# Performance work log

Hardware: AMD Instinct MI355X
Metric: run time of the kernel (lower is better)

The kernel has to match this reference:

```python
import jax, jax.numpy as jnp
import numpy as np

D_MODEL = 1024
NUM_HEADS = 16
D_K = D_MODEL // NUM_HEADS


def setup_inputs() -> dict:
    key = jax.random.key(0)
    ks = jax.random.split(key, 11)
    B, S, D = 2, 2048, D_MODEL
    scale = 1.0 / np.sqrt(D)
    inp = {
        'q': jax.random.normal(ks[0], (B, S, D), jnp.float32),
        'k': jax.random.normal(ks[1], (B, S, D), jnp.float32),
        'v': jax.random.normal(ks[2], (B, S, D), jnp.float32),
        # torch nn.Linear weights are [out, in]; y = x @ W.T + b
        'Wq': jax.random.normal(ks[3], (D, D), jnp.float32) * scale,
        'bq': jax.random.normal(ks[4], (D,), jnp.float32) * scale,
        'Wk': jax.random.normal(ks[5], (D, D), jnp.float32) * scale,
        'bk': jax.random.normal(ks[6], (D,), jnp.float32) * scale,
        'Wv': jax.random.normal(ks[7], (D, D), jnp.float32) * scale,
        'bv': jax.random.normal(ks[8], (D,), jnp.float32) * scale,
        'Wo': jax.random.normal(ks[9], (D, D), jnp.float32) * scale,
        'bo': jax.random.normal(ks[10], (D,), jnp.float32) * scale,
    }
    return inp


def reference(q, k, v, Wq, bq, Wk, bk, Wv, bv, Wo, bo):
    B, S, D = q.shape
    H, dk = NUM_HEADS, D_K

    def proj(x, W, b):
        # torch Linear: x @ W.T + b ; then [B,S,H,dk] -> [B,H,S,dk]
        y = jnp.einsum('bsd,ed->bse', x, W) + b
        return y.reshape(B, S, H, dk).transpose(0, 2, 1, 3)

    Q = proj(q, Wq, bq)
    K = proj(k, Wk, bk)
    V = proj(v, Wv, bv)

    # NOTE: original module omits the 1/sqrt(d_k) scaling — faithful here.
    scores = jnp.einsum('bhqd,bhkd->bhqk', Q, K)  # [B,H,S,S]
    attn = jax.nn.softmax(scores, axis=-1)
    out = jnp.einsum('bhqk,bhkd->bhqd', attn, V)  # [B,H,S,dk]
    out = out.transpose(0, 2, 1, 3).reshape(B, S, D)
    return jnp.einsum('bsd,ed->bse', out, Wo) + bo
```

## Files before the change

kernel.cpp:

```cpp
#include <hip/hip_runtime.h>
#include <hip/hip_bf16.h>
#include <stdint.h>


using bf16 = __hip_bfloat16;
typedef __attribute__((ext_vector_type(8))) short v8s;
typedef __attribute__((ext_vector_type(4))) float v4f;

#define NB_ ((size_t)4194304)
#define ND_ ((size_t)1048576)

__device__ __forceinline__ void async16(const void* g, void* l) {
  __builtin_amdgcn_global_load_lds(
      (const __attribute__((address_space(1))) unsigned int*)g,
      (__attribute__((address_space(3))) unsigned int*)l, 16, 0, 0);
}

__device__ __forceinline__ v4f mfma16(v8s a, v8s b, v4f c) {
  return __builtin_amdgcn_mfma_f32_16x16x32_bf16(a, b, c, 0, 0, 0);
}

struct SplitArgs {
  const float4* src[7];
  ushort4* hi[7];
  ushort4* lo[7];
  int n4[7];
};

__global__ __launch_bounds__(256) void splitk(SplitArgs sa) {
  const int z = blockIdx.y;
  const float4* __restrict__ src = sa.src[z];
  ushort4* __restrict__ dh = sa.hi[z];
  ushort4* __restrict__ dl = sa.lo[z];
  const int n4 = sa.n4[z];
  const int stride = gridDim.x * blockDim.x;
  for (int i = blockIdx.x * blockDim.x + threadIdx.x; i < n4; i += stride) {
    const float4 x = src[i];
    float vals[4] = {x.x, x.y, x.z, x.w};
    unsigned short hs[4], ls[4];
#pragma unroll
    for (int j = 0; j < 4; ++j) {
      bf16 hb = __float2bfloat16(vals[j]);
      float rest = vals[j] - __bfloat162float(hb);
      bf16 lb = __float2bfloat16(rest);
      __builtin_memcpy(&hs[j], &hb, 2);
      __builtin_memcpy(&ls[j], &lb, 2);
    }
    ushort4 hv; hv.x = hs[0]; hv.y = hs[1]; hv.z = hs[2]; hv.w = hs[3];
    ushort4 lv; lv.x = ls[0]; lv.y = ls[1]; lv.z = ls[2]; lv.w = ls[3];
    dh[i] = hv;
    dl[i] = lv;
  }
}

struct GemmArgs {
  const bf16* Ah[3];
  const bf16* Al[3];
  const bf16* Bh[3];
  const bf16* Bl[3];
  const float* bias[3];
  void* O0[3];
  void* O1[3];
  int mode[3];
};

template <int TM>
__global__ __launch_bounds__(256, TM == 128 ? 3 : 2) void gemm3t(GemmArgs ga) {
  constexpr int MFR = TM / 32;
  const int z = blockIdx.z;
  const bf16* __restrict__ Ah = ga.Ah[z];
  const bf16* __restrict__ Al = ga.Al[z];
  const bf16* __restrict__ Bh = ga.Bh[z];
  const bf16* __restrict__ Bl = ga.Bl[z];
  const float* __restrict__ bias = ga.bias[z];
  const int mode = ga.mode[z];

  __shared__ alignas(16) bf16 lA0[TM * 32];
  __shared__ alignas(16) bf16 lA1[TM * 32];
  __shared__ alignas(16) bf16 lB0[128 * 32];
  __shared__ alignas(16) bf16 lB1[128 * 32];

  const int tid = threadIdx.x;
  const int lane = tid & 63;
  const int w = tid >> 6, wr = w >> 1, wc = w & 1;
  const int ln = lane & 15, g = lane >> 4;
  const int h4 = g * 4;
  const int m0 = blockIdx.y * TM, n0 = blockIdx.x * 128;

  v4f acc[MFR][4];
#pragma unroll
  for (int i = 0; i < MFR; ++i)
#pragma unroll
    for (int j = 0; j < 4; ++j)
#pragma unroll
      for (int r = 0; r < 4; ++r) acc[i][j][r] = 0.f;

  for (int k0 = 0; k0 < 1024; k0 += 32) {
#pragma unroll
    for (int p = 0; p < TM / 64; ++p) {
      const int idx = p * 256 + tid;
      const int row = idx >> 2, c = idx & 3;
      const int cs = (c ^ (row & 3)) * 8;
      const size_t gA = (size_t)(m0 + row) * 1024 + k0 + cs;
      async16(Ah + gA, &lA0[idx * 8]);
      async16(Al + gA, &lA1[idx * 8]);
    }
#pragma unroll
    for (int p = 0; p < 2; ++p) {
      const int idx = p * 256 + tid;
      const int row = idx >> 2, c = idx & 3;
      const int cs = (c ^ (row & 3)) * 8;
      const size_t gB = (size_t)(n0 + row) * 1024 + k0 + cs;
      async16(Bh + gB, &lB0[idx * 8]);
      async16(Bl + gB, &lB1[idx * 8]);
    }
    __syncthreads();

    const char* pA0 = (const char*)lA0;
    const char* pA1 = (const char*)lA1;
    const char* pB0 = (const char*)lB0;
    const char* pB1 = (const char*)lB1;

    v8s a0[MFR], a1[MFR], b0[4], b1[4];
#pragma unroll
    for (int f = 0; f < MFR; ++f) {
      const int row = wr * (TM / 2) + f * 16 + ln;
      const int off = (row << 6) + ((g ^ (row & 3)) << 4);
      a0[f] = *(const v8s*)(pA0 + off);
      a1[f] = *(const v8s*)(pA1 + off);
    }
#pragma unroll
    for (int f = 0; f < 4; ++f) {
      const int row = wc * 64 + f * 16 + ln;
      const int off = (row << 6) + ((g ^ (row & 3)) << 4);
      b0[f] = *(const v8s*)(pB0 + off);
      b1[f] = *(const v8s*)(pB1 + off);
    }
    __builtin_amdgcn_s_setprio(1);
#pragma unroll
    for (int i = 0; i < MFR; ++i)
#pragma unroll
      for (int j = 0; j < 4; ++j) {
        acc[i][j] = mfma16(a0[i], b0[j], acc[i][j]);
        acc[i][j] = mfma16(a0[i], b1[j], acc[i][j]);
        acc[i][j] = mfma16(a1[i], b0[j], acc[i][j]);
      }
    __builtin_amdgcn_s_setprio(0);
    __syncthreads();
  }

#pragma unroll
  for (int i = 0; i < MFR; ++i)
#pragma unroll
    for (int j = 0; j < 4; ++j) {
      const int col = n0 + wc * 64 + j * 16 + ln;
      const float bb = bias[col];
#pragma unroll
      for (int r = 0; r < 4; ++r) {
        const int row = m0 + wr * (TM / 2) + i * 16 + h4 + r;
        const float vv = acc[i][j][r] + bb;
        if (mode == 2) {
          ((float*)ga.O0[z])[(size_t)row * 1024 + col] = vv;
        } else {
          const int b_ = row >> 11, s_ = row & 2047;
          const int hh = col >> 6, dd = col & 63;
          if (mode == 0) {
            const size_t o = (((size_t)(b_ * 16 + hh)) * 2048 + s_) * 64 + dd;
            bf16 hb = __float2bfloat16(vv);
            ((bf16*)ga.O0[z])[o] = hb;
            ((bf16*)ga.O1[z])[o] = __float2bfloat16(vv - __bfloat162float(hb));
          } else {
            const size_t o = (((size_t)(b_ * 16 + hh)) * 64 + dd) * 2048 + s_;
            ((bf16*)ga.O0[z])[o] = __float2bfloat16(vv);
          }
        }
      }
    }
}

__global__ __launch_bounds__(256, 2) void attnk(
    const bf16* __restrict__ Qh, const bf16* __restrict__ Ql,
    const bf16* __restrict__ Kh, const bf16* __restrict__ Kl,
    const bf16* __restrict__ Vt,
    bf16* __restrict__ Oh, bf16* __restrict__ Ol) {
  __shared__ alignas(16) bf16 lKh[2][64 * 64];
  __shared__ alignas(16) bf16 lKl[2][64 * 64];
  __shared__ alignas(16) bf16 lVt[2][64 * 64];
  __shared__ alignas(16) bf16 lP[4][32 * 72];

  const int tid = threadIdx.x;
  const int lane = tid & 63, w = tid >> 6;
  const int ln = lane & 15, g = lane >> 4;
  const int h8 = g * 8, h4 = g * 4;
  const int bh = blockIdx.y;
  const int q0 = blockIdx.x * 128 + w * 32;

  v8s qh[2][2], ql[2][2];
#pragma unroll
  for (int mf = 0; mf < 2; ++mf) {
    const size_t rowg = (size_t)bh * 2048 + q0 + mf * 16 + ln;
#pragma unroll
    for (int ks = 0; ks < 2; ++ks) {
      qh[mf][ks] = *(const v8s*)&Qh[rowg * 64 + ks * 32 + h8];
      ql[mf][ks] = *(const v8s*)&Ql[rowg * 64 + ks * 32 + h8];
    }
  }

  v4f O[2][4];
  float lpart[2][4];
#pragma unroll
  for (int mf = 0; mf < 2; ++mf) {
#pragma unroll
    for (int r = 0; r < 4; ++r) lpart[mf][r] = 0.f;
#pragma unroll
    for (int d = 0; d < 4; ++d)
#pragma unroll
      for (int r = 0; r < 4; ++r) O[mf][d][r] = 0.f;
  }

  auto stage = [&](int buf, int kv0) {
#pragma unroll
    for (int p = 0; p < 2; ++p) {
      const int idx = p * 256 + tid;
      const int row = idx >> 3;
      const int cs = ((idx & 7) ^ (row & 7)) * 8;
      const size_t gk = ((size_t)bh * 2048 + kv0 + row) * 64 + cs;
      async16(Kh + gk, &lKh[buf][idx * 8]);
      async16(Kl + gk, &lKl[buf][idx * 8]);
      const size_t gv = ((size_t)bh * 64 + row) * 2048 + kv0 + cs;
      async16(Vt + gv, &lVt[buf][idx * 8]);
    }
  };

  stage(0, 0);
  __syncthreads();

  for (int t = 0; t < 32; ++t) {
    const int cur = t & 1;
    if (t < 31) stage(cur ^ 1, (t + 1) * 64);

    v4f sacc[2][4];
#pragma unroll
    for (int mf = 0; mf < 2; ++mf)
#pragma unroll
      for (int kvf = 0; kvf < 4; ++kvf)
#pragma unroll
        for (int r = 0; r < 4; ++r) sacc[mf][kvf][r] = 0.f;

    const char* kbh = (const char*)&lKh[cur][0];
    const char* kbl = (const char*)&lKl[cur][0];
    const char* vbb = (const char*)&lVt[cur][0];

#pragma unroll
    for (int ks = 0; ks < 2; ++ks) {
      const int cbyte = (ks << 6) + (g << 4);
      v8s kh[4], kl[4];
#pragma unroll
      for (int kvf = 0; kvf < 4; ++kvf) {
        const int kr = kvf * 16 + ln;
        const int koff = (kr << 7) + (cbyte ^ ((kr & 7) << 4));
        kh[kvf] = *(const v8s*)(kbh + koff);
        kl[kvf] = *(const v8s*)(kbl + koff);
      }
      __builtin_amdgcn_s_setprio(1);
#pragma unroll
      for (int mf = 0; mf < 2; ++mf)
#pragma unroll
        for (int kvf = 0; kvf < 4; ++kvf) {
          sacc[mf][kvf] = mfma16(qh[mf][ks], kh[kvf], sacc[mf][kvf]);
          sacc[mf][kvf] = mfma16(qh[mf][ks], kl[kvf], sacc[mf][kvf]);
          sacc[mf][kvf] = mfma16(ql[mf][ks], kh[kvf], sacc[mf][kvf]);
        }
      __builtin_amdgcn_s_setprio(0);
    }

#pragma unroll
    for (int mf = 0; mf < 2; ++mf)
#pragma unroll
      for (int kvf = 0; kvf < 4; ++kvf)
#pragma unroll
        for (int r = 0; r < 4; ++r) {
          const float p = __expf(sacc[mf][kvf][r]);
          lpart[mf][r] += p;
          lP[w][(mf * 16 + h4 + r) * 72 + kvf * 16 + ln] = __float2bfloat16(p);
        }

#pragma unroll
    for (int ks = 0; ks < 2; ++ks) {
      const int cbyte = (ks << 6) + (g << 4);
      v8s pa[2], vb[4];
#pragma unroll
      for (int mf = 0; mf < 2; ++mf)
        pa[mf] = *(const v8s*)&lP[w][(mf * 16 + ln) * 72 + ks * 32 + h8];
#pragma unroll
      for (int dkf = 0; dkf < 4; ++dkf) {
        const int vr = dkf * 16 + ln;
        const int voff = (vr << 7) + (cbyte ^ ((vr & 7) << 4));
        vb[dkf] = *(const v8s*)(vbb + voff);
      }
      __builtin_amdgcn_s_setprio(1);
#pragma unroll
      for (int mf = 0; mf < 2; ++mf)
#pragma unroll
        for (int dkf = 0; dkf < 4; ++dkf)
          O[mf][dkf] = mfma16(pa[mf], vb[dkf], O[mf][dkf]);
      __builtin_amdgcn_s_setprio(0);
    }
    __syncthreads();
  }

  float lrow[2][4];
#pragma unroll
  for (int mf = 0; mf < 2; ++mf)
#pragma unroll
    for (int r = 0; r < 4; ++r) {
      float s = lpart[mf][r];
      s += __shfl_xor(s, 1, 64);
      s += __shfl_xor(s, 2, 64);
      s += __shfl_xor(s, 4, 64);
      s += __shfl_xor(s, 8, 64);
      lrow[mf][r] = s;
    }

  const int b_ = bh >> 4, hh = bh & 15;
#pragma unroll
  for (int mf = 0; mf < 2; ++mf)
#pragma unroll
    for (int r = 0; r < 4; ++r) {
      const float inv = 1.f / lrow[mf][r];
      const int s_ = blockIdx.x * 128 + w * 32 + mf * 16 + h4 + r;
#pragma unroll
      for (int dkf = 0; dkf < 4; ++dkf) {
        const float o = O[mf][dkf][r] * inv;
        const size_t off = ((size_t)b_ * 2048 + s_) * 1024 + hh * 64 + dkf * 16 + ln;
        bf16 hb = __float2bfloat16(o);
        Oh[off] = hb;
        Ol[off] = __float2bfloat16(o - __bfloat162float(hb));
      }
    }
}

extern "C" void kernel_launch(void* const* d_in, const int* in_sizes, int n_in,
                              void* d_out, int out_size, void* d_ws, size_t ws_size,
                              hipStream_t stream) {
  const float* q  = (const float*)d_in[0];
  const float* k  = (const float*)d_in[1];
  const float* v  = (const float*)d_in[2];
  const float* Wq = (const float*)d_in[3];
  const float* bq = (const float*)d_in[4];
  const float* Wk = (const float*)d_in[5];
  const float* bk = (const float*)d_in[6];
  const float* Wv = (const float*)d_in[7];
  const float* bv = (const float*)d_in[8];
  const float* Wo = (const float*)d_in[9];
  const float* bo = (const float*)d_in[10];

  const size_t NB = NB_, ND = ND_;
  bf16* P = (bf16*)d_ws;

  const bool fused = (ws_size >= (size_t)120 * 1024 * 1024);

  if (fused) {
    bf16 *qh = P, *ql = qh + NB, *kh = ql + NB, *kl = kh + NB, *vh = kl + NB, *vl = vh + NB;
    bf16 *wqh = vl + NB, *wql = wqh + ND, *wkh = wql + ND, *wkl = wkh + ND;
    bf16 *wvh = wkl + ND, *wvl = wvh + ND, *woh = wvl + ND, *wol = woh + ND;
    bf16 *Qh = wol + ND, *Ql = Qh + NB, *Kh2 = Ql + NB, *Kl2 = Kh2 + NB, *Vt = Kl2 + NB;
    bf16 *Ah = qh, *Al = ql;

    SplitArgs sa{};
    const float* srcs[7] = {q, k, v, Wq, Wk, Wv, Wo};
    bf16* his[7] = {qh, kh, vh, wqh, wkh, wvh, woh};
    bf16* los[7] = {ql, kl, vl, wql, wkl, wvl, wol};
    for (int i = 0; i < 7; ++i) {
      sa.src[i] = (const float4*)srcs[i];
      sa.hi[i] = (ushort4*)his[i];
      sa.lo[i] = (ushort4*)los[i];
      sa.n4[i] = (int)((i < 3 ? NB : ND) / 4);
    }
    splitk<<<dim3(512, 7), 256, 0, stream>>>(sa);

    GemmArgs ga{};
    ga.Ah[0] = qh; ga.Al[0] = ql; ga.Bh[0] = wqh; ga.Bl[0] = wql;
    ga.bias[0] = bq; ga.O0[0] = Qh; ga.O1[0] = Ql; ga.mode[0] = 0;
    ga.Ah[1] = kh; ga.Al[1] = kl; ga.Bh[1] = wkh; ga.Bl[1] = wkl;
    ga.bias[1] = bk; ga.O0[1] = Kh2; ga.O1[1] = Kl2; ga.mode[1] = 0;
    ga.Ah[2] = vh; ga.Al[2] = vl; ga.Bh[2] = wvh; ga.Bl[2] = wvl;
    ga.bias[2] = bv; ga.O0[2] = Vt; ga.O1[2] = nullptr; ga.mode[2] = 1;
    gemm3t<128><<<dim3(8, 32, 3), 256, 0, stream>>>(ga);

    attnk<<<dim3(16, 32), 256, 0, stream>>>(Qh, Ql, Kh2, Kl2, Vt, Ah, Al);

    GemmArgs go{};
    go.Ah[0] = Ah; go.Al[0] = Al; go.Bh[0] = woh; go.Bl[0] = wol;
    go.bias[0] = bo; go.O0[0] = d_out; go.O1[0] = nullptr; go.mode[0] = 2;
    gemm3t<64><<<dim3(8, 64, 1), 256, 0, stream>>>(go);
  } else {
    bf16 *ash = P, *asl = ash + NB, *wsh = asl + NB, *wsl = wsh + ND;
    bf16 *Qh = wsl + ND, *Ql = Qh + NB, *Kh2 = Ql + NB, *Kl2 = Kh2 + NB, *Vt = Kl2 + NB;

    auto do_split2 = [&](const float* a, const float* wsrc) {
      SplitArgs s{};
      s.src[0] = (const float4*)a; s.hi[0] = (ushort4*)ash; s.lo[0] = (ushort4*)asl;
      s.n4[0] = (int)(NB / 4);
      s.src[1] = (const float4*)wsrc; s.hi[1] = (ushort4*)wsh; s.lo[1] = (ushort4*)wsl;
      s.n4[1] = (int)(ND / 4);
      splitk<<<dim3(512, 2), 256, 0, stream>>>(s);
    };
    auto do_gemm = [&](const float* bias, void* o0, void* o1, int mode) {
      GemmArgs g{};
      g.Ah[0] = ash; g.Al[0] = asl; g.Bh[0] = wsh; g.Bl[0] = wsl;
      g.bias[0] = bias; g.O0[0] = o0; g.O1[0] = o1; g.mode[0] = mode;
      gemm3t<128><<<dim3(8, 32, 1), 256, 0, stream>>>(g);
    };

    do_split2(q, Wq); do_gemm(bq, Qh, Ql, 0);
    do_split2(k, Wk); do_gemm(bk, Kh2, Kl2, 0);
    do_split2(v, Wv); do_gemm(bv, Vt, nullptr, 1);

    attnk<<<dim3(16, 32), 256, 0, stream>>>(Qh, Ql, Kh2, Kl2, Vt, ash, asl);

    SplitArgs s4{};
    s4.src[0] = (const float4*)Wo; s4.hi[0] = (ushort4*)wsh; s4.lo[0] = (ushort4*)wsl;
    s4.n4[0] = (int)(ND / 4);
    splitk<<<dim3(512, 1), 256, 0, stream>>>(s4);
    GemmArgs g4{};
    g4.Ah[0] = ash; g4.Al[0] = asl; g4.Bh[0] = wsh; g4.Bl[0] = wsl;
    g4.bias[0] = bo; g4.O0[0] = d_out; g4.O1[0] = nullptr; g4.mode[0] = 2;
    gemm3t<64><<<dim3(8, 64, 1), 256, 0, stream>>>(g4);
  }
}
```

Measured before the change: 325.0 us.

## Restructure attention to 16-row waves with register-shuffled P; drop weight-lo term in V/O GEMMs

The attention kernel now uses 512 threads, with each wave owning 16 query rows instead of 32. It computes S transposed (K as the A operand), so the exponentiated probabilities can be passed into the PV MFMA through cross-lane shuffles rather than an LDS round-trip, and the per-wave P buffer in shared memory is gone. This is meant to cut LDS traffic and register pressure and to raise occupancy. Separately, the GEMM gains a per-problem term count, so the V projection and output projection skip the A_hi*B_lo MFMA and its weight-lo load, trading a small amount of precision for fewer MFMAs and less bandwidth.

```diff
diff --git a/kernel.cpp b/kernel.cpp
--- a/kernel.cpp
+++ b/kernel.cpp
@@ -6,6 +6,8 @@
 using bf16 = __hip_bfloat16;
 typedef __attribute__((ext_vector_type(8))) short v8s;
 typedef __attribute__((ext_vector_type(4))) float v4f;
+typedef __attribute__((ext_vector_type(4))) unsigned int v4u;
+union PW { v4u u; v8s s; };
 
 #define NB_ ((size_t)4194304)
 #define ND_ ((size_t)1048576)
@@ -18,6 +20,13 @@
 
 __device__ __forceinline__ v4f mfma16(v8s a, v8s b, v4f c) {
   return __builtin_amdgcn_mfma_f32_16x16x32_bf16(a, b, c, 0, 0, 0);
+}
+
+__device__ __forceinline__ unsigned short bfbits(float x) {
+  bf16 h = __float2bfloat16(x);
+  unsigned short u;
+  __builtin_memcpy(&u, &h, 2);
+  return u;
 }
 
 struct SplitArgs {
@@ -42,9 +51,8 @@
     for (int j = 0; j < 4; ++j) {
       bf16 hb = __float2bfloat16(vals[j]);
       float rest = vals[j] - __bfloat162float(hb);
-      bf16 lb = __float2bfloat16(rest);
-      __builtin_memcpy(&hs[j], &hb, 2);
-      __builtin_memcpy(&ls[j], &lb, 2);
+      hs[j] = bfbits(vals[j]);
+      ls[j] = bfbits(rest);
     }
     ushort4 hv; hv.x = hs[0]; hv.y = hs[1]; hv.z = hs[2]; hv.w = hs[3];
     ushort4 lv; lv.x = ls[0]; lv.y = ls[1]; lv.z = ls[2]; lv.w = ls[3];
@@ -62,6 +70,7 @@
   void* O0[3];
   void* O1[3];
   int mode[3];
+  int terms[3];
 };
 
 template <int TM>
@@ -74,6 +83,7 @@
   const bf16* __restrict__ Bl = ga.Bl[z];
   const float* __restrict__ bias = ga.bias[z];
   const int mode = ga.mode[z];
+  const bool nt3 = (ga.terms[z] == 3);
 
   __shared__ alignas(16) bf16 lA0[TM * 32];
   __shared__ alignas(16) bf16 lA1[TM * 32];
@@ -112,7 +122,7 @@
       const int cs = (c ^ (row & 3)) * 8;
       const size_t gB = (size_t)(n0 + row) * 1024 + k0 + cs;
       async16(Bh + gB, &lB0[idx * 8]);
-      async16(Bl + gB, &lB1[idx * 8]);
+      if (nt3) async16(Bl + gB, &lB1[idx * 8]);
     }
     __syncthreads();
 
@@ -134,7 +144,14 @@
       const int row = wc * 64 + f * 16 + ln;
       const int off = (row << 6) + ((g ^ (row & 3)) << 4);
       b0[f] = *(const v8s*)(pB0 + off);
-      b1[f] = *(const v8s*)(pB1 + off);
+    }
+    if (nt3) {
+#pragma unroll
+      for (int f = 0; f < 4; ++f) {
+        const int row = wc * 64 + f * 16 + ln;
+        const int off = (row << 6) + ((g ^ (row & 3)) << 4);
+        b1[f] = *(const v8s*)(pB1 + off);
+      }
     }
     __builtin_amdgcn_s_setprio(1);
 #pragma unroll
@@ -142,9 +159,15 @@
 #pragma unroll
       for (int j = 0; j < 4; ++j) {
         acc[i][j] = mfma16(a0[i], b0[j], acc[i][j]);
-        acc[i][j] = mfma16(a0[i], b1[j], acc[i][j]);
         acc[i][j] = mfma16(a1[i], b0[j], acc[i][j]);
       }
+    if (nt3) {
+#pragma unroll
+      for (int i = 0; i < MFR; ++i)
+#pragma unroll
+        for (int j = 0; j < 4; ++j)
+          acc[i][j] = mfma16(a0[i], b1[j], acc[i][j]);
+    }
     __builtin_amdgcn_s_setprio(0);
     __syncthreads();
   }
@@ -178,7 +201,7 @@
     }
 }
 
-__global__ __launch_bounds__(256, 2) void attnk(
+__global__ __launch_bounds__(512, 4) void attnk(
     const bf16* __restrict__ Qh, const bf16* __restrict__ Ql,
     const bf16* __restrict__ Kh, const bf16* __restrict__ Kl,
     const bf16* __restrict__ Vt,
@@ -186,70 +209,59 @@
   __shared__ alignas(16) bf16 lKh[2][64 * 64];
   __shared__ alignas(16) bf16 lKl[2][64 * 64];
   __shared__ alignas(16) bf16 lVt[2][64 * 64];
-  __shared__ alignas(16) bf16 lP[4][32 * 72];
 
   const int tid = threadIdx.x;
   const int lane = tid & 63, w = tid >> 6;
   const int ln = lane & 15, g = lane >> 4;
-  const int h8 = g * 8, h4 = g * 4;
+  const int h8 = g * 8;
   const int bh = blockIdx.y;
-  const int q0 = blockIdx.x * 128 + w * 32;
-
-  v8s qh[2][2], ql[2][2];
-#pragma unroll
-  for (int mf = 0; mf < 2; ++mf) {
-    const size_t rowg = (size_t)bh * 2048 + q0 + mf * 16 + ln;
-#pragma unroll
-    for (int ks = 0; ks < 2; ++ks) {
-      qh[mf][ks] = *(const v8s*)&Qh[rowg * 64 + ks * 32 + h8];
-      ql[mf][ks] = *(const v8s*)&Ql[rowg * 64 + ks * 32 + h8];
-    }
-  }
-
-  v4f O[2][4];
-  float lpart[2][4];
-#pragma unroll
-  for (int mf = 0; mf < 2; ++mf) {
-#pragma unroll
-    for (int r = 0; r < 4; ++r) lpart[mf][r] = 0.f;
-#pragma unroll
-    for (int d = 0; d < 4; ++d)
-#pragma unroll
-      for (int r = 0; r < 4; ++r) O[mf][d][r] = 0.f;
-  }
-
+  const int q0 = blockIdx.x * 128 + w * 16;
+
+  v8s qh[2], ql[2];
+  {
+    const size_t rowg = (size_t)bh * 2048 + q0 + ln;
+    qh[0] = *(const v8s*)&Qh[rowg * 64 + h8];
+    qh[1] = *(const v8s*)&Qh[rowg * 64 + 32 + h8];
+    ql[0] = *(const v8s*)&Ql[rowg * 64 + h8];
+    ql[1] = *(const v8s*)&Ql[rowg * 64 + 32 + h8];
+  }
+
+  v4f O[4];
+  float lpart = 0.f;
+#pragma unroll
+  for (int d = 0; d < 4; ++d)
+#pragma unroll
+    for (int r = 0; r < 4; ++r) O[d][r] = 0.f;
+
+  const int srow = tid >> 3, sc = tid & 7;
+  const int scs = (sc ^ (srow & 7)) * 8;
   auto stage = [&](int buf, int kv0) {
-#pragma unroll
-    for (int p = 0; p < 2; ++p) {
-      const int idx = p * 256 + tid;
-      const int row = idx >> 3;
-      const int cs = ((idx & 7) ^ (row & 7)) * 8;
-      const size_t gk = ((size_t)bh * 2048 + kv0 + row) * 64 + cs;
-      async16(Kh + gk, &lKh[buf][idx * 8]);
-      async16(Kl + gk, &lKl[buf][idx * 8]);
-      const size_t gv = ((size_t)bh * 64 + row) * 2048 + kv0 + cs;
-      async16(Vt + gv, &lVt[buf][idx * 8]);
-    }
+    const size_t gk = ((size_t)bh * 2048 + kv0 + srow) * 64 + scs;
+    async16(Kh + gk, &lKh[buf][tid * 8]);
+    async16(Kl + gk, &lKl[buf][tid * 8]);
+    const size_t gv = ((size_t)bh * 64 + srow) * 2048 + kv0 + scs;
+    async16(Vt + gv, &lVt[buf][tid * 8]);
   };
 
   stage(0, 0);
   __syncthreads();
+
+  const int sA = ln + ((g & 1) << 5);
+  const bool hiK = (g >> 1) != 0;
 
   for (int t = 0; t < 32; ++t) {
     const int cur = t & 1;
     if (t < 31) stage(cur ^ 1, (t + 1) * 64);
 
-    v4f sacc[2][4];
-#pragma unroll
-    for (int mf = 0; mf < 2; ++mf)
-#pragma unroll
-      for (int kvf = 0; kvf < 4; ++kvf)
-#pragma unroll
-        for (int r = 0; r < 4; ++r) sacc[mf][kvf][r] = 0.f;
-
     const char* kbh = (const char*)&lKh[cur][0];
     const char* kbl = (const char*)&lKl[cur][0];
     const char* vbb = (const char*)&lVt[cur][0];
+
+    v4f sacc[4];
+#pragma unroll
+    for (int kvf = 0; kvf < 4; ++kvf)
+#pragma unroll
+      for (int r = 0; r < 4; ++r) sacc[kvf][r] = 0.f;
 
 #pragma unroll
     for (int ks = 0; ks < 2; ++ks) {
@@ -264,34 +276,42 @@
       }
       __builtin_amdgcn_s_setprio(1);
 #pragma unroll
-      for (int mf = 0; mf < 2; ++mf)
-#pragma unroll
-        for (int kvf = 0; kvf < 4; ++kvf) {
-          sacc[mf][kvf] = mfma16(qh[mf][ks], kh[kvf], sacc[mf][kvf]);
-          sacc[mf][kvf] = mfma16(qh[mf][ks], kl[kvf], sacc[mf][kvf]);
-          sacc[mf][kvf] = mfma16(ql[mf][ks], kh[kvf], sacc[mf][kvf]);
-        }
+      for (int kvf = 0; kvf < 4; ++kvf) {
+        sacc[kvf] = mfma16(kh[kvf], qh[ks], sacc[kvf]);
+        sacc[kvf] = mfma16(kl[kvf], qh[ks], sacc[kvf]);
+        sacc[kvf] = mfma16(kh[kvf], ql[ks], sacc[kvf]);
+      }
       __builtin_amdgcn_s_setprio(0);
     }
 
-#pragma unroll
-    for (int mf = 0; mf < 2; ++mf)
-#pragma unroll
-      for (int kvf = 0; kvf < 4; ++kvf)
-#pragma unroll
-        for (int r = 0; r < 4; ++r) {
-          const float p = __expf(sacc[mf][kvf][r]);
-          lpart[mf][r] += p;
-          lP[w][(mf * 16 + h4 + r) * 72 + kvf * 16 + ln] = __float2bfloat16(p);
-        }
+    unsigned wb[4][2];
+#pragma unroll
+    for (int kvf = 0; kvf < 4; ++kvf) {
+      const float p0 = __expf(sacc[kvf][0]);
+      const float p1 = __expf(sacc[kvf][1]);
+      const float p2 = __expf(sacc[kvf][2]);
+      const float p3 = __expf(sacc[kvf][3]);
+      lpart += (p0 + p1) + (p2 + p3);
+      wb[kvf][0] = (unsigned)bfbits(p0) | ((unsigned)bfbits(p1) << 16);
+      wb[kvf][1] = (unsigned)bfbits(p2) | ((unsigned)bfbits(p3) << 16);
+    }
 
 #pragma unroll
     for (int ks = 0; ks < 2; ++ks) {
+      const unsigned a0 = __shfl(wb[2 * ks][0], sA, 64);
+      const unsigned b0 = __shfl(wb[2 * ks + 1][0], sA, 64);
+      const unsigned a1 = __shfl(wb[2 * ks][1], sA, 64);
+      const unsigned b1 = __shfl(wb[2 * ks + 1][1], sA, 64);
+      const unsigned a2 = __shfl(wb[2 * ks][0], sA + 16, 64);
+      const unsigned b2 = __shfl(wb[2 * ks + 1][0], sA + 16, 64);
+      const unsigned a3 = __shfl(wb[2 * ks][1], sA + 16, 64);
+      const unsigned b3 = __shfl(wb[2 * ks + 1][1], sA + 16, 64);
+      PW pw;
+      pw.u = (v4u){hiK ? b0 : a0, hiK ? b1 : a1, hiK ? b2 : a2, hiK ? b3 : a3};
+      const v8s pa = pw.s;
+
       const int cbyte = (ks << 6) + (g << 4);
-      v8s pa[2], vb[4];
-#pragma unroll
-      for (int mf = 0; mf < 2; ++mf)
-        pa[mf] = *(const v8s*)&lP[w][(mf * 16 + ln) * 72 + ks * 32 + h8];
+      v8s vb[4];
 #pragma unroll
       for (int dkf = 0; dkf < 4; ++dkf) {
         const int vr = dkf * 16 + ln;
@@ -300,44 +320,32 @@
       }
       __builtin_amdgcn_s_setprio(1);
 #pragma unroll
-      for (int mf = 0; mf < 2; ++mf)
-#pragma unroll
-        for (int dkf = 0; dkf < 4; ++dkf)
-          O[mf][dkf] = mfma16(pa[mf], vb[dkf], O[mf][dkf]);
+      for (int dkf = 0; dkf < 4; ++dkf)
+        O[dkf] = mfma16(pa, vb[dkf], O[dkf]);
       __builtin_amdgcn_s_setprio(0);
     }
     __syncthreads();
   }
 
-  float lrow[2][4];
-#pragma unroll
-  for (int mf = 0; mf < 2; ++mf)
-#pragma unroll
-    for (int r = 0; r < 4; ++r) {
-      float s = lpart[mf][r];
-      s += __shfl_xor(s, 1, 64);
-      s += __shfl_xor(s, 2, 64);
-      s += __shfl_xor(s, 4, 64);
-      s += __shfl_xor(s, 8, 64);
-      lrow[mf][r] = s;
-    }
+  float s = lpart;
+  s += __shfl_xor(s, 16, 64);
+  s += __shfl_xor(s, 32, 64);
+  const float sinv = 1.f / s;
 
   const int b_ = bh >> 4, hh = bh & 15;
 #pragma unroll
-  for (int mf = 0; mf < 2; ++mf)
-#pragma unroll
-    for (int r = 0; r < 4; ++r) {
-      const float inv = 1.f / lrow[mf][r];
-      const int s_ = blockIdx.x * 128 + w * 32 + mf * 16 + h4 + r;
-#pragma unroll
-      for (int dkf = 0; dkf < 4; ++dkf) {
-        const float o = O[mf][dkf][r] * inv;
-        const size_t off = ((size_t)b_ * 2048 + s_) * 1024 + hh * 64 + dkf * 16 + ln;
-        bf16 hb = __float2bfloat16(o);
-        Oh[off] = hb;
-        Ol[off] = __float2bfloat16(o - __bfloat162float(hb));
-      }
-    }
+  for (int r = 0; r < 4; ++r) {
+    const float inv = __shfl(sinv, g * 4 + r, 64);
+    const int s_ = blockIdx.x * 128 + w * 16 + g * 4 + r;
+#pragma unroll
+    for (int dkf = 0; dkf < 4; ++dkf) {
+      const float o = O[dkf][r] * inv;
+      const size_t off = ((size_t)b_ * 2048 + s_) * 1024 + hh * 64 + dkf * 16 + ln;
+      bf16 hb = __float2bfloat16(o);
+      Oh[off] = hb;
+      Ol[off] = __float2bfloat16(o - __bfloat162float(hb));
+    }
+  }
 }
 
 extern "C" void kernel_launch(void* const* d_in, const int* in_sizes, int n_in,
@@ -381,18 +389,18 @@
 
     GemmArgs ga{};
     ga.Ah[0] = qh; ga.Al[0] = ql; ga.Bh[0] = wqh; ga.Bl[0] = wql;
-    ga.bias[0] = bq; ga.O0[0] = Qh; ga.O1[0] = Ql; ga.mode[0] = 0;
+    ga.bias[0] = bq; ga.O0[0] = Qh; ga.O1[0] = Ql; ga.mode[0] = 0; ga.terms[0] = 3;
     ga.Ah[1] = kh; ga.Al[1] = kl; ga.Bh[1] = wkh; ga.Bl[1] = wkl;
-    ga.bias[1] = bk; ga.O0[1] = Kh2; ga.O1[1] = Kl2; ga.mode[1] = 0;
+    ga.bias[1] = bk; ga.O0[1] = Kh2; ga.O1[1] = Kl2; ga.mode[1] = 0; ga.terms[1] = 3;
     ga.Ah[2] = vh; ga.Al[2] = vl; ga.Bh[2] = wvh; ga.Bl[2] = wvl;
-    ga.bias[2] = bv; ga.O0[2] = Vt; ga.O1[2] = nullptr; ga.mode[2] = 1;
+    ga.bias[2] = bv; ga.O0[2] = Vt; ga.O1[2] = nullptr; ga.mode[2] = 1; ga.terms[2] = 2;
     gemm3t<128><<<dim3(8, 32, 3), 256, 0, stream>>>(ga);
 
-    attnk<<<dim3(16, 32), 256, 0, stream>>>(Qh, Ql, Kh2, Kl2, Vt, Ah, Al);
+    attnk<<<dim3(16, 32), 512, 0, stream>>>(Qh, Ql, Kh2, Kl2, Vt, Ah, Al);
 
     GemmArgs go{};
     go.Ah[0] = Ah; go.Al[0] = Al; go.Bh[0] = woh; go.Bl[0] = wol;
-    go.bias[0] = bo; go.O0[0] = d_out; go.O1[0] = nullptr; go.mode[0] = 2;
+    go.bias[0] = bo; go.O0[0] = d_out; go.O1[0] = nullptr; go.mode[0] = 2; go.terms[0] = 2;
     gemm3t<64><<<dim3(8, 64, 1), 256, 0, stream>>>(go);
   } else {
     bf16 *ash = P, *asl = ash + NB, *wsh = asl + NB, *wsl = wsh + ND;
@@ -406,18 +414,18 @@
       s.n4[1] = (int)(ND / 4);
       splitk<<<dim3(512, 2), 256, 0, stream>>>(s);
     };
-    auto do_gemm = [&](const float* bias, void* o0, void* o1, int mode) {
+    auto do_gemm = [&](const float* bias, void* o0, void* o1, int mode, int terms) {
       GemmArgs g{};
       g.Ah[0] = ash; g.Al[0] = asl; g.Bh[0] = wsh; g.Bl[0] = wsl;
-      g.bias[0] = bias; g.O0[0] = o0; g.O1[0] = o1; g.mode[0] = mode;
+      g.bias[0] = bias; g.O0[0] = o0; g.O1[0] = o1; g.mode[0] = mode; g.terms[0] = terms;
       gemm3t<128><<<dim3(8, 32, 1), 256, 0, stream>>>(g);
     };
 
-    do_split2(q, Wq); do_gemm(bq, Qh, Ql, 0);
-    do_split2(k, Wk); do_gemm(bk, Kh2, Kl2, 0);
-    do_split2(v, Wv); do_gemm(bv, Vt, nullptr, 1);
-
-    attnk<<<dim3(16, 32), 256, 0, stream>>>(Qh, Ql, Kh2, Kl2, Vt, ash, asl);
+    do_split2(q, Wq); do_gemm(bq, Qh, Ql, 0, 3);
+    do_split2(k, Wk); do_gemm(bk, Kh2, Kl2, 0, 3);
+    do_split2(v, Wv); do_gemm(bv, Vt, nullptr, 1, 2);
+
+    attnk<<<dim3(16, 32), 512, 0, stream>>>(Qh, Ql, Kh2, Kl2, Vt, ash, asl);
 
     SplitArgs s4{};
     s4.src[0] = (const float4*)Wo; s4.hi[0] = (ushort4*)wsh; s4.lo[0] = (ushort4*)wsl;
@@ -425,7 +433,7 @@
     splitk<<<dim3(512, 1), 256, 0, stream>>>(s4);
     GemmArgs g4{};
     g4.Ah[0] = ash; g4.Al[0] = asl; g4.Bh[0] = wsh; g4.Bl[0] = wsl;
-    g4.bias[0] = bo; g4.O0[0] = d_out; g4.O1[0] = nullptr; g4.mode[0] = 2;
+    g4.bias[0] = bo; g4.O0[0] = d_out; g4.O1[0] = nullptr; g4.mode[0] = 2; g4.terms[0] = 2;
     gemm3t<64><<<dim3(8, 64, 1), 256, 0, stream>>>(g4);
   }
 }
```

Measured after the change: 315.5 us. 2.9% less time.
